# Optimization experiments

Measured on AMD Instinct MI355X. Metric: run time of the kernel, lower is better.

The kernel has to match this reference:

```python
import jax, jax.numpy as jnp
import numpy as np

BS, T, NN, NF = 4, 64, 128, 16
HID, HEADS, RH, LD = 64, 4, 256, 64
EPG = 1024  # edges per graph


def _gat(x, src, dst, N, W, a_s, a_d, b, heads, out_dim, concat):
    # x: [N, Fin] -> h: [N, H, F]
    h = (x @ W).reshape(N, heads, out_dim)
    al_s = jnp.sum(h * a_s[None], axis=-1)  # [N, H]
    al_d = jnp.sum(h * a_d[None], axis=-1)
    e = jax.nn.leaky_relu(al_s[src] + al_d[dst], 0.2)  # [E, H]
    m = jax.ops.segment_max(e, dst, num_segments=N)
    m = jnp.where(jnp.isfinite(m), m, 0.0)
    ex = jnp.exp(e - m[dst])
    den = jax.ops.segment_sum(ex, dst, num_segments=N)
    alpha = ex / (den[dst] + 1e-16)
    agg = jax.ops.segment_sum(h[src] * alpha[:, :, None], dst, num_segments=N)
    o = agg.reshape(N, heads * out_dim) if concat else agg.mean(axis=1)
    return o + b


def _lstm(xs, Wih, Whh, bih, bhh, H):
    # xs: [T, B, D]; PyTorch gate order i,f,g,o
    B = xs.shape[1]
    h0 = jnp.zeros((B, H), xs.dtype)
    c0 = jnp.zeros((B, H), xs.dtype)

    def step(carry, xt):
        h, c = carry
        g = xt @ Wih.T + h @ Whh.T + bih + bhh
        i, f, gg, o = jnp.split(g, 4, axis=-1)
        c = jax.nn.sigmoid(f) * c + jax.nn.sigmoid(i) * jnp.tanh(gg)
        h = jax.nn.sigmoid(o) * jnp.tanh(c)
        return (h, c), None

    (hT, _), _ = jax.lax.scan(step, (h0, c0), xs)
    return hT


def setup_inputs() -> dict:
    key = jax.random.key(0)
    ks = jax.random.split(key, 32)
    s = 0.1
    d = {
        'x': jax.random.normal(ks[0], (BS, T, NN, NF), jnp.float32),
        'edge_index': jax.random.randint(ks[1], (2, EPG), 0, NN),
        'gat0_W': s * jax.random.normal(ks[2], (NF, HEADS * HID)),
        'gat0_asrc': s * jax.random.normal(ks[3], (HEADS, HID)),
        'gat0_adst': s * jax.random.normal(ks[4], (HEADS, HID)),
        'gat0_b': jnp.zeros((HEADS * HID,)),
        'gat1_W': s * jax.random.normal(ks[5], (HEADS * HID, HEADS * HID)),
        'gat1_asrc': s * jax.random.normal(ks[6], (HEADS, HID)),
        'gat1_adst': s * jax.random.normal(ks[7], (HEADS, HID)),
        'gat1_b': jnp.zeros((HEADS * HID,)),
        'gat2_W': s * jax.random.normal(ks[8], (HEADS * HID, HID)),
        'gat2_asrc': s * jax.random.normal(ks[9], (1, HID)),
        'gat2_adst': s * jax.random.normal(ks[10], (1, HID)),
        'gat2_b': jnp.zeros((HID,)),
        'Wih_f': s * jax.random.normal(ks[11], (4 * RH, HID)),
        'Whh_f': s * jax.random.normal(ks[12], (4 * RH, RH)),
        'bih_f': jnp.zeros((4 * RH,)),
        'bhh_f': jnp.zeros((4 * RH,)),
        'Wih_b': s * jax.random.normal(ks[13], (4 * RH, HID)),
        'Whh_b': s * jax.random.normal(ks[14], (4 * RH, RH)),
        'bih_b': jnp.zeros((4 * RH,)),
        'bhh_b': jnp.zeros((4 * RH,)),
        'mu_W': s * jax.random.normal(ks[15], (LD, 2 * RH)),
        'mu_b': jnp.zeros((LD,)),
        'lv_W': s * jax.random.normal(ks[16], (LD, 2 * RH)),
        'lv_b': jnp.zeros((LD,)),
    }
    return d


def reference(x, edge_index, gat0_W, gat0_asrc, gat0_adst, gat0_b,
              gat1_W, gat1_asrc, gat1_adst, gat1_b,
              gat2_W, gat2_asrc, gat2_adst, gat2_b,
              Wih_f, Whh_f, bih_f, bhh_f, Wih_b, Whh_b, bih_b, bhh_b,
              mu_W, mu_b, lv_W, lv_b):
    bs, t, nn, nf = x.shape
    ng = bs * t
    N = ng * nn
    xt = x.reshape(N, nf)
    # batch the edge index: repeat per graph with node offset, then add self-loops
    off = (jnp.arange(ng) * nn).repeat(edge_index.shape[1])  # [ng*E]
    bsrc = jnp.tile(edge_index[0], ng) + off
    bdst = jnp.tile(edge_index[1], ng) + off
    loops = jnp.arange(N)
    src = jnp.concatenate([bsrc, loops])
    dst = jnp.concatenate([bdst, loops])

    xt = jax.nn.relu(_gat(xt, src, dst, N, gat0_W, gat0_asrc, gat0_adst, gat0_b, HEADS, HID, True))
    xt = jax.nn.relu(_gat(xt, src, dst, N, gat1_W, gat1_asrc, gat1_adst, gat1_b, HEADS, HID, True))
    xt = jax.nn.relu(_gat(xt, src, dst, N, gat2_W, gat2_asrc, gat2_adst, gat2_b, 1, HID, False))

    batch_idx = jnp.arange(ng).repeat(nn)
    graph_embs = jax.ops.segment_sum(xt, batch_idx, num_segments=ng).reshape(bs, t, HID)

    seq = jnp.transpose(graph_embs, (1, 0, 2))  # [T, B, HID]
    h_fwd = _lstm(seq, Wih_f, Whh_f, bih_f, bhh_f, RH)
    h_bwd = _lstm(seq[::-1], Wih_b, Whh_b, bih_b, bhh_b, RH)
    feat = jnp.concatenate([h_fwd, h_bwd], axis=1)  # [B, 2*RH]

    mu = feat @ mu_W.T + mu_b
    logvar = feat @ lv_W.T + lv_b
    # PoincareBall(c=1).projx, float32 eps = 4e-3
    maxnorm = 1.0 - 4e-3
    nrm = jnp.linalg.norm(mu, axis=-1, keepdims=True)
    mu = jnp.where(nrm > maxnorm, mu / nrm * maxnorm, mu)
    return (mu, logvar)
```

## Files before the change

kernel.cpp:

```cpp
#include <hip/hip_runtime.h>
#include <hip/hip_bf16.h>

#define BSZ 4
#define TT 64
#define NNODE 128
#define NFEAT 16
#define HIDD 64
#define NHEAD 4
#define RHID 256
#define LDIM 64
#define EPG 1024
#define NGRAPH (BSZ*TT)
#define NTOT (NGRAPH*NNODE)
#define ESLOTS (EPG+NNODE)

#define WOFF_G0W 0
#define WOFF_G0AS 4096
#define WOFF_G0AD 4352
#define WOFF_G0B 4608
#define WOFF_G1W 4864
#define WOFF_G1AS 70400
#define WOFF_G1AD 70656
#define WOFF_G1B 70912
#define WOFF_G2W 71168
#define WOFF_G2AS 87552
#define WOFF_G2AD 87616
#define WOFF_G2B 87680
#define WOFF_WIHF 87744
#define WOFF_WHHF 153280
#define WOFF_BIHF 415424
#define WOFF_BHHF 416448
#define WOFF_WIHB 417472
#define WOFF_WHHB 483008
#define WOFF_BIHB 745152
#define WOFF_BHHB 746176
#define WOFF_MUW 747200
#define WOFF_MUB 779968
#define WOFF_LVW 780032
#define WOFF_LVB 812800
#define WTOTAL   812864

#define FOFF_WBUF 4096
#define FOFF_CSR  1052672
#define FOFF_SYNC 1314816
#define FOFF_WE   1576960
#define FOFF_BBF  1900000
#define FOFF_XFP  2756608
#define FOFF_XBP  3018752
#define FOFF_HT   3280896
#define FOFF_XSEQ 3282944
#define FOFF_PA   3291136
#define FOFF_PB   5388288
#define FOFF_P    7485440

#define BOFF_G0 0
#define BOFF_G1 4096
#define BOFF_G2 69632
#define BOFF_WF 86016
#define BOFF_WB 151552
#define BTOTAL  217088

#define SP_CVTX  (WTOTAL + BTOTAL)
#define SP_WHH   (SP_CVTX + NTOT*NFEAT)
#define SP_HX    (SP_WHH + 262144)
#define SP_FL    (SP_HX + 12288)
#define SP_TOTAL (SP_FL + 1024)

#define SENT 0xFFFFFFFFu

typedef __attribute__((ext_vector_type(8))) short short8;
typedef __attribute__((ext_vector_type(4))) float float4v;

__device__ __forceinline__ float b2f(unsigned short u){
  union { unsigned int i; float f; } v; v.i = ((unsigned int)u) << 16; return v.f;
}
__device__ __forceinline__ unsigned short f2b(float f){
  __hip_bfloat16 h = __float2bfloat16(f);
  union { __hip_bfloat16 h; unsigned short u; } v; v.h = h; return v.u;
}
__device__ __forceinline__ float ldf(const void* p, int i, int flag){
  return flag ? b2f(((const unsigned short*)p)[i]) : ((const float*)p)[i];
}
__device__ __forceinline__ float h2f(unsigned short s){
  union { _Float16 hh; unsigned short s; } u; u.s = s; return (float)u.hh;
}
__device__ __forceinline__ unsigned short f2h(float f){
  union { _Float16 hh; unsigned short s; } u; u.hh = (_Float16)f; return u.s;
}
__device__ __forceinline__ int sniff32(const unsigned short* w){
  int ok = 0;
  #pragma unroll
  for (int i = 0; i < 32; ++i){
    float a = fabsf(b2f(w[2 * i]));
    if (a > 1e-8f && a < 4.f) ok++;
  }
  return ok >= 16 ? 1 : 0;
}

struct CvtArgs {
  const void* src[24];
  int off[25];
};
__global__ void setup_kernel(CvtArgs a,
                             float* __restrict__ W, unsigned short* __restrict__ BBF,
                             unsigned short* __restrict__ P, unsigned int* __restrict__ WT,
                             unsigned int* __restrict__ HX, int* __restrict__ FL,
                             const void* __restrict__ x, const int* __restrict__ ei,
                             int* __restrict__ csr_row, unsigned short* __restrict__ csr_src)
{
  __shared__ int cnt[NNODE];
  __shared__ int off[NNODE];
  __shared__ int wo[NNODE];
  const int tid = threadIdx.x;

  if (blockIdx.x == gridDim.x - 1){
    if (tid < NNODE) cnt[tid] = 0;
    __syncthreads();
    for (int i = tid; i < ESLOTS; i += 256){
      int d = (i < EPG) ? ei[EPG + i] : (i - EPG);
      atomicAdd(&cnt[d], 1);
    }
    __syncthreads();
    if (tid < NNODE) off[tid] = cnt[tid];
    for (int o = 1; o < NNODE; o <<= 1){
      __syncthreads();
      int t = (tid < NNODE && tid >= o) ? off[tid - o] : 0;
      __syncthreads();
      if (tid < NNODE) off[tid] += t;
    }
    __syncthreads();
    if (tid < NNODE){
      wo[tid] = off[tid] - cnt[tid];
      csr_row[tid + 1] = off[tid];
    }
    if (tid == 0) csr_row[0] = 0;
    __syncthreads();
    for (int i = tid; i < ESLOTS; i += 256){
      int s, d;
      if (i < EPG){ s = ei[i]; d = ei[EPG + i]; } else { s = i - EPG; d = i - EPG; }
      int pos = atomicAdd(&wo[d], 1);
      csr_src[pos] = (unsigned short)s;
    }
    return;
  }

  int id = blockIdx.x * blockDim.x + tid;
  if (id >= SP_TOTAL) return;
  int fl = sniff32((const unsigned short*)a.src[0]);
  if (id < WTOTAL){
    int k = 0;
    while (id >= a.off[k + 1]) ++k;
    W[id] = ldf(a.src[k], id - a.off[k], fl);
  } else if (id < WTOTAL + BTOTAL){
    int r = id - WTOTAL;
    float v;
    if (r < BOFF_G1){
      int o = r >> 4, k = r & 15;
      v = ldf(a.src[0], k * 256 + o, fl);
    } else if (r < BOFF_G2){
      int rr = r - BOFF_G1; int o = rr >> 8, k = rr & 255;
      v = ldf(a.src[4], k * 256 + o, fl);
    } else if (r < BOFF_WF){
      int rr = r - BOFF_G2; int o = rr >> 8, k = rr & 255;
      v = ldf(a.src[8], k * 64 + o, fl);
    } else if (r < BOFF_WB){
      int q = r - BOFF_WF; int k = q >> 10, n = q & 1023;
      v = ldf(a.src[12], n * 64 + k, fl);
    } else {
      int q = r - BOFF_WB; int k = q >> 10, n = q & 1023;
      v = ldf(a.src[16], n * 64 + k, fl);
    }
    BBF[r] = f2b(v);
  } else if (id < SP_CVTX + NTOT * NFEAT){
    int r = id - SP_CVTX;
    P[r] = fl ? ((const unsigned short*)x)[r] : f2b(((const float*)x)[r]);
  } else if (id < SP_HX){
    int r0 = id - SP_WHH;
    int c = r0 & 3;
    int lane = (r0 >> 2) & 63;
    int nt = (r0 >> 8) & 15;
    int kc = (r0 >> 12) & 7;
    int m = (r0 >> 15) & 3;
    int dir = r0 >> 17;
    int l = nt * 16 + (lane & 15);
    int u = (l >> 6) * 256 + 64 * m + (l & 63);
    int k0 = kc * 32 + ((lane >> 4) << 3) + 2 * c;
    const void* Wsrc = dir ? a.src[17] : a.src[13];
    unsigned short va = f2b(ldf(Wsrc, u * RHID + k0, fl));
    unsigned short vb = f2b(ldf(Wsrc, u * RHID + k0 + 1, fl));
    WT[r0] = (unsigned int)va | ((unsigned int)vb << 16);
  } else if (id < SP_FL){
    HX[id - SP_HX] = SENT;
  } else {
    FL[id - SP_FL] = 0;
  }
}

__global__ __launch_bounds__(256)
void gat3_kernel(const unsigned short* Pb, const unsigned short* BBF,
                 const float* Wbuf,
                 const int* csr_row, const unsigned short* csr_src,
                 unsigned short* PA, unsigned short* PB,
                 unsigned short* XSEQ, int* FL)
{
  __shared__ unsigned short HT_[128 * 136];
  __shared__ unsigned short AD[128 * 136];
  __shared__ unsigned short ALS16[256];
  __shared__ unsigned short ALD16[256];
  __shared__ float ALSf[128];
  __shared__ float ALDf[128];
  __shared__ int   rowL[132];
  __shared__ unsigned char srcL[1152];
  __shared__ float pools[4][64];

  const int tid = threadIdx.x;
  const int g = blockIdx.x >> 1, hb = blockIdx.x & 1;
  const int c0 = hb * 128;
  const int w = tid >> 6, lane = tid & 63, q = lane >> 4, r = lane & 15;
  unsigned short* Bst = AD;

  for (int i = tid; i < 129; i += 256) rowL[i] = csr_row[i];
  for (int i = tid; i < 1152; i += 256) srcL[i] = (unsigned char)csr_src[i];
  __syncthreads();

  auto gemm_T = [&](int KV, int NT, const unsigned short* Pin, const unsigned short* BT){
    float4v acc0[8], acc1[8];
    #pragma unroll
    for (int i = 0; i < 8; ++i){ acc0[i] = (float4v){0,0,0,0}; acc1[i] = (float4v){0,0,0,0}; }
    const int cbase = (NT == 8) ? c0 : 0;
    const int KR = (KV + 31) / 32;
    for (int kr = 0; kr < KR; ++kr){
      const int kc = kr * 32;
      __syncthreads();
      if (NT == 8){
        int n = tid >> 1, kb = (tid & 1) * 16;
        uint4 z = {0,0,0,0}; uint4 v0 = z, v1 = z;
        if (kb < KV)     v0 = *(const uint4*)(BT + (size_t)(cbase + n) * KV + kc + kb);
        if (kb + 8 < KV) v1 = *(const uint4*)(BT + (size_t)(cbase + n) * KV + kc + kb + 8);
        *(uint4*)&Bst[n * 40 + kb] = v0;
        *(uint4*)&Bst[n * 40 + kb + 8] = v1;
      } else {
        int n = tid >> 2, kb = (tid & 3) * 8;
        uint4 v = *(const uint4*)(BT + (size_t)n * KV + kc + kb);
        *(uint4*)&Bst[n * 40 + kb] = v;
      }
      short8 a0 = {0,0,0,0,0,0,0,0}, a1 = {0,0,0,0,0,0,0,0};
      if (KV >= 32 || q < 2){
        a0 = *(const short8*)(Pin + (size_t)(g * 128 + 16 * w       + r) * KV + kc + q * 8);
        a1 = *(const short8*)(Pin + (size_t)(g * 128 + 16 * (w + 4) + r) * KV + kc + q * 8);
      }
      __syncthreads();
      for (int nt = 0; nt < NT; ++nt){
        short8 bf = *(const short8*)&Bst[(16 * nt + r) * 40 + q * 8];
        acc0[nt] = __builtin_amdgcn_mfma_f32_16x16x32_bf16(a0, bf, acc0[nt], 0, 0, 0);
        acc1[nt] = __builtin_amdgcn_mfma_f32_16x16x32_bf16(a1, bf, acc1[nt], 0, 0, 0);
      }
    }
    __syncthreads();
    for (int nt = 0; nt < NT; ++nt)
      #pragma unroll
      for (int i = 0; i < 4; ++i){
        HT_[(16 * nt + r) * 136 + 16 * w       + q * 4 + i] = f2b(acc0[nt][i]);
        HT_[(16 * nt + r) * 136 + 16 * (w + 4) + q * 4 + i] = f2b(acc1[nt][i]);
      }
    __syncthreads();
  };

  auto agg_head = [&](int hl, int colbase, float4v am[2][4]){
    #pragma unroll
    for (int mt = 0; mt < 2; ++mt)
      #pragma unroll
      for (int nt = 0; nt < 4; ++nt) am[mt][nt] = (float4v){0,0,0,0};
    #pragma unroll
    for (int kc = 0; kc < 4; ++kc){
      short8 af0 = *(const short8*)&AD[(w * 32      + r) * 136 + kc * 32 + q * 8];
      short8 af1 = *(const short8*)&AD[(w * 32 + 16 + r) * 136 + kc * 32 + q * 8];
      #pragma unroll
      for (int nt = 0; nt < 4; ++nt){
        short8 bf = *(const short8*)&HT_[(colbase + nt * 16 + r) * 136 + kc * 32 + q * 8];
        am[0][nt] = __builtin_amdgcn_mfma_f32_16x16x32_bf16(af0, bf, am[0][nt], 0, 0, 0);
        am[1][nt] = __builtin_amdgcn_mfma_f32_16x16x32_bf16(af1, bf, am[1][nt], 0, 0, 0);
      }
    }
  };

  auto sync_partner = [&](int* FLx){
    __syncthreads();
    if (tid == 0){
      __hip_atomic_store(&FLx[blockIdx.x], 1, __ATOMIC_RELEASE, __HIP_MEMORY_SCOPE_AGENT);
      int guard = 0;
      while (__hip_atomic_load(&FLx[blockIdx.x ^ 1], __ATOMIC_ACQUIRE,
                               __HIP_MEMORY_SCOPE_AGENT) == 0 && guard < 200000){
        __builtin_amdgcn_s_sleep(1);
        ++guard;
      }
    }
    __syncthreads();
  };

  auto do_layer = [&](int KV, const unsigned short* Pin, const unsigned short* BT,
                      int asoff, int adoff, int boff, unsigned short* Pout){
    gemm_T(KV, 8, Pin, BT);
    {
      float as0 = Wbuf[asoff + c0 + 2 * lane], as1 = Wbuf[asoff + c0 + 2 * lane + 1];
      float ad0 = Wbuf[adoff + c0 + 2 * lane], ad1 = Wbuf[adoff + c0 + 2 * lane + 1];
      for (int it = 0; it < 32; ++it){
        int n = it * 4 + w;
        float e0 = b2f(HT_[(2 * lane) * 136 + n]);
        float e1 = b2f(HT_[(2 * lane + 1) * 136 + n]);
        float vs = e0 * as0 + e1 * as1;
        float vd = e0 * ad0 + e1 * ad1;
        #pragma unroll
        for (int m = 16; m >= 1; m >>= 1){ vs += __shfl_xor(vs, m); vd += __shfl_xor(vd, m); }
        if ((lane & 31) == 0){
          ALS16[n * 2 + (lane >> 5)] = f2h(vs);
          ALD16[n * 2 + (lane >> 5)] = f2h(vd);
        }
      }
    }
    __syncthreads();
    for (int hl = 0; hl < 2; ++hl){
      for (int i = tid; i < 8704; i += 256) ((unsigned int*)AD)[i] = 0;
      __syncthreads();
      if (tid < 128){
        int n = tid;
        float aldv = h2f(ALD16[n * 2 + hl]);
        int rs = rowL[n], re = rowL[n + 1];
        float mx = -3e38f, den = 0.f;
        for (int j = rs; j < re; ++j){
          float v = h2f(ALS16[srcL[j] * 2 + hl]) + aldv;
          v = v > 0.f ? v : 0.2f * v;
          if (v > mx){ den = den * __expf(mx - v) + 1.f; mx = v; }
          else den += __expf(v - mx);
        }
        float iden = 1.f / (den + 1e-16f);
        for (int j = rs; j < re; ++j){
          float v = h2f(ALS16[srcL[j] * 2 + hl]) + aldv;
          v = v > 0.f ? v : 0.2f * v;
          float al = __expf(v - mx) * iden;
          int s = srcL[j];
          AD[n * 136 + s] = f2b(b2f(AD[n * 136 + s]) + al);
        }
      }
      __syncthreads();
      float4v am[2][4];
      agg_head(hl, hl * 64, am);
      #pragma unroll
      for (int mt = 0; mt < 2; ++mt)
        #pragma unroll
        for (int nt = 0; nt < 4; ++nt){
          int col = hl * 64 + nt * 16 + r;
          float bz = Wbuf[boff + c0 + col];
          #pragma unroll
          for (int i = 0; i < 4; ++i){
            int dst = w * 32 + mt * 16 + q * 4 + i;
            float v = am[mt][nt][i] + bz;
            v = v > 0.f ? v : 0.f;
            __hip_atomic_store((unsigned short*)&Pout[(size_t)(g * 128 + dst) * 256 + c0 + col],
                               f2b(v), __ATOMIC_RELAXED, __HIP_MEMORY_SCOPE_AGENT);
          }
        }
      __syncthreads();
    }
  };

  do_layer(16, Pb, BBF + BOFF_G0, WOFF_G0AS, WOFF_G0AD, WOFF_G0B, PA);
  sync_partner(FL);
  do_layer(256, PA, BBF + BOFF_G1, WOFF_G1AS, WOFF_G1AD, WOFF_G1B, PB);
  sync_partner(FL + 512);

  {
    gemm_T(256, 4, PB, BBF + BOFF_G2);
    {
      float asv = Wbuf[WOFF_G2AS + lane];
      float adv = Wbuf[WOFF_G2AD + lane];
      for (int it = 0; it < 32; ++it){
        int n = it * 4 + w;
        float e0 = b2f(HT_[lane * 136 + n]);
        float vs = e0 * asv, vd = e0 * adv;
        #pragma unroll
        for (int m = 32; m >= 1; m >>= 1){ vs += __shfl_xor(vs, m); vd += __shfl_xor(vd, m); }
        if (lane == 0){ ALSf[n] = vs; ALDf[n] = vd; }
      }
    }
    __syncthreads();
    for (int i = tid; i < 8704; i += 256) ((unsigned int*)AD)[i] = 0;
    __syncthreads();
    if (tid < 128){
      int n = tid;
      float aldv = ALDf[n];
      int rs = rowL[n], re = rowL[n + 1];
      float mx = -3e38f, den = 0.f;
      for (int j = rs; j < re; ++j){
        float v = ALSf[srcL[j]] + aldv;
        v = v > 0.f ? v : 0.2f * v;
        if (v > mx){ den = den * __expf(mx - v) + 1.f; mx = v; }
        else den += __expf(v - mx);
      }
      float iden = 1.f / (den + 1e-16f);
      for (int j = rs; j < re; ++j){
        float v = ALSf[srcL[j]] + aldv;
        v = v > 0.f ? v : 0.2f * v;
        float al = __expf(v - mx) * iden;
        int s = srcL[j];
        AD[n * 136 + s] = f2b(b2f(AD[n * 136 + s]) + al);
      }
    }
    __syncthreads();
    float4v am[2][4];
    agg_head(0, 0, am);
    float psum[4] = {0.f, 0.f, 0.f, 0.f};
    #pragma unroll
    for (int nt = 0; nt < 4; ++nt){
      int col = nt * 16 + r;
      float bz = Wbuf[WOFF_G2B + col];
      #pragma unroll
      for (int mt = 0; mt < 2; ++mt)
        #pragma unroll
        for (int i = 0; i < 4; ++i){
          float v = am[mt][nt][i] + bz;
          psum[nt] += (v > 0.f ? v : 0.f);
        }
      psum[nt] += __shfl_xor(psum[nt], 16);
      psum[nt] += __shfl_xor(psum[nt], 32);
    }
    if (q == 0){
      #pragma unroll
      for (int nt = 0; nt < 4; ++nt) pools[w][nt * 16 + r] = psum[nt];
    }
    __syncthreads();
    if (tid < 64 && (tid >> 5) == hb){
      float s = pools[0][tid] + pools[1][tid] + pools[2][tid] + pools[3][tid];
      int b = g >> 6, tq = g & 63;
      XSEQ[(size_t)(tq * BSZ + b) * HIDD + tid] = f2b(s);
    }
  }
}

__global__ __launch_bounds__(256)
void mmx2_kernel(const unsigned short* __restrict__ A,
                 const unsigned short* __restrict__ B0, const unsigned short* __restrict__ B1,
                 float* __restrict__ C0, float* __restrict__ C1, int M, int Nc, int K)
{
  __shared__ unsigned short As[64][40];
  __shared__ unsigned short Bs[64][40];
  const unsigned short* Bb = blockIdx.z ? B1 : B0;
  float* C = blockIdx.z ? C1 : C0;
  const int tid = threadIdx.x;
  const int w = tid >> 6, lane = tid & 63, q = lane >> 4, r = lane & 15;
  const int m0 = blockIdx.x * 64, n0 = blockIdx.y * 64;
  float4v acc0 = {0,0,0,0}, acc1 = {0,0,0,0}, acc2 = {0,0,0,0}, acc3 = {0,0,0,0};
  const int arow = tid >> 2, akb = (tid & 3) * 8;
  const int bk = tid >> 3, bnb = (tid & 7) * 8;
  for (int kc = 0; kc < K; kc += 32){
    int kw = K - kc; if (kw > 32) kw = 32;
    if (akb < kw){
      uint4 v = *(const uint4*)(A + (size_t)(m0 + arow) * K + kc + akb);
      *(uint4*)&As[arow][akb] = v;
    } else {
      uint4 z = {0,0,0,0}; *(uint4*)&As[arow][akb] = z;
    }
    if (bk < kw){
      uint4 v = *(const uint4*)(Bb + (size_t)(kc + bk) * Nc + n0 + bnb);
      const unsigned short* vs = (const unsigned short*)&v;
      #pragma unroll
      for (int e = 0; e < 8; ++e) Bs[bnb + e][bk] = vs[e];
    } else {
      #pragma unroll
      for (int e = 0; e < 8; ++e) Bs[bnb + e][bk] = 0;
    }
    __syncthreads();
    short8 af = *(const short8*)&As[16 * w + r][q * 8];
    short8 b0 = *(const short8*)&Bs[r][q * 8];
    short8 b1 = *(const short8*)&Bs[16 + r][q * 8];
    short8 b2 = *(const short8*)&Bs[32 + r][q * 8];
    short8 b3 = *(const short8*)&Bs[48 + r][q * 8];
    acc0 = __builtin_amdgcn_mfma_f32_16x16x32_bf16(af, b0, acc0, 0, 0, 0);
    acc1 = __builtin_amdgcn_mfma_f32_16x16x32_bf16(af, b1, acc1, 0, 0, 0);
    acc2 = __builtin_amdgcn_mfma_f32_16x16x32_bf16(af, b2, acc2, 0, 0, 0);
    acc3 = __builtin_amdgcn_mfma_f32_16x16x32_bf16(af, b3, acc3, 0, 0, 0);
    __syncthreads();
  }
  const int row = m0 + 16 * w + q * 4, col0 = n0 + r;
  #pragma unroll
  for (int i = 0; i < 4; ++i){
    size_t base = (size_t)(row + i) * Nc;
    C[base + col0]      = acc0[i];
    C[base + col0 + 16] = acc1[i];
    C[base + col0 + 32] = acc2[i];
    C[base + col0 + 48] = acc3[i];
  }
}

__global__ __launch_bounds__(256)
void lstm13_kernel(const float* __restrict__ XF, const float* __restrict__ XB,
                   const unsigned int* __restrict__ WT,
                   const float* __restrict__ bih_f, const float* __restrict__ bhh_f,
                   const float* __restrict__ bih_b, const float* __restrict__ bhh_b,
                   unsigned int* __restrict__ HX,
                   float* __restrict__ HT)
{
  __shared__ unsigned int WL[32768];
  __shared__ unsigned int H16[16 * 132];
  __shared__ float glds[4][256];

  const int tid = threadIdx.x;
  const int m = blockIdx.x & 3, dir = blockIdx.x >> 2;
  const int w = tid >> 6, lane = tid & 63, quad = lane >> 4, r = lane & 15;
  const float* Xp = dir ? XB : XF;
  const int ub = tid >> 6, uj = tid & 63;
  unsigned int* HXd = HX + dir * 6144;

  const float* bi = dir ? bih_b : bih_f;
  const float* bh = dir ? bhh_b : bhh_f;
  float bias0 = bi[0 * 256 + 64 * m + uj] + bh[0 * 256 + 64 * m + uj];
  float bias1 = bi[1 * 256 + 64 * m + uj] + bh[1 * 256 + 64 * m + uj];
  float bias2 = bi[2 * 256 + 64 * m + uj] + bh[2 * 256 + 64 * m + uj];
  float bias3 = bi[3 * 256 + 64 * m + uj] + bh[3 * 256 + 64 * m + uj];

  {
    const uint4* WT4 = (const uint4*)(WT + dir * 131072 + m * 32768);
    uint4* WL4 = (uint4*)WL;
    #pragma unroll
    for (int s = 0; s < 32; ++s)
      WL4[s * 256 + tid] = WT4[s * 256 + tid];
  }
  for (int i = tid; i < 16 * 132; i += 256) H16[i] = 0;
  float c = 0.f;
  __syncthreads();

  const uint4* WL4 = (const uint4*)WL;
  const uint4* H16u4 = (const uint4*)H16;

  float4v acc[4];
  auto kchunk = [&](int kc){
    uint4 av = H16u4[(lane & 15) * 33 + kc * 4 + quad];
    short8 af = *(const short8*)&av;
    #pragma unroll
    for (int t = 0; t < 4; ++t){
      int nt = w * 4 + t;
      uint4 bv = WL4[(kc * 16 + nt) * 64 + lane];
      short8 bf = *(const short8*)&bv;
      acc[t] = __builtin_amdgcn_mfma_f32_16x16x32_bf16(af, bf, acc[t], 0, 0, 0);
    }
  };

  for (int t = 0; t < TT; ++t){
    const int tb = dir ? (TT - 1 - t) : t;
    const float* xr = Xp + (size_t)(tb * 4 + ub) * 1024 + 64 * m + uj;
    float x0 = xr[0], x1 = xr[256], x2 = xr[512], x3 = xr[768];

    #pragma unroll
    for (int i = 0; i < 4; ++i) acc[i] = (float4v){0,0,0,0};
    kchunk(2 * m); kchunk(2 * m + 1);
    if (t > 0 && w > 0){
      int qp = (m + w) & 3;
      unsigned int* S = HXd + ((t - 1) % 3) * 2048 + m * 512;
      int b2 = lane >> 5, p2 = lane & 31;
      int i1G = b2 * 128 + 32 * qp + p2;
      int i2G = (b2 + 2) * 128 + 32 * qp + p2;
      int i1L = b2 * 132 + 32 * qp + p2;
      int i2L = (b2 + 2) * 132 + 32 * qp + p2;
      unsigned int v1, v2;
      int guard = 0;
      while ((v1 = __hip_atomic_load(&S[i1G], __ATOMIC_RELAXED, __HIP_MEMORY_SCOPE_AGENT)) == SENT
             && guard < 200000){ __builtin_amdgcn_s_sleep(1); ++guard; }
      guard = 0;
      while ((v2 = __hip_atomic_load(&S[i2G], __ATOMIC_RELAXED, __HIP_MEMORY_SCOPE_AGENT)) == SENT
             && guard < 200000){ __builtin_amdgcn_s_sleep(1); ++guard; }
      H16[i1L] = v1; H16[i2L] = v2;
      __hip_atomic_store(&S[i1G], SENT, __ATOMIC_RELAXED, __HIP_MEMORY_SCOPE_AGENT);
      __hip_atomic_store(&S[i2G], SENT, __ATOMIC_RELAXED, __HIP_MEMORY_SCOPE_AGENT);
    }
    __syncthreads();
    #pragma unroll
    for (int i = 1; i < 4; ++i){
      int qp = (m + i) & 3;
      kchunk(2 * qp); kchunk(2 * qp + 1);
    }
    if (quad == 0){
      #pragma unroll
      for (int tt = 0; tt < 4; ++tt){
        int l = (w * 4 + tt) * 16 + r;
        glds[0][l] = acc[tt][0];
        glds[1][l] = acc[tt][1];
        glds[2][l] = acc[tt][2];
        glds[3][l] = acc[tt][3];
      }
    }
    __syncthreads();

    float gi = glds[ub][uj]        + bias0 + x0;
    float gf = glds[ub][64 + uj]   + bias1 + x1;
    float gg = glds[ub][128 + uj]  + bias2 + x2;
    float go = glds[ub][192 + uj]  + bias3 + x3;
    float si = 1.f / (1.f + __expf(-gi));
    float sf = 1.f / (1.f + __expf(-gf));
    float so = 1.f / (1.f + __expf(-go));
    float tg = 1.f - 2.f / (1.f + __expf(2.f * gg));
    c = sf * c + si * tg;
    float ch = 1.f - 2.f / (1.f + __expf(2.f * c));
    float hval = so * ch;
    if (t == TT - 1){
      HT[(size_t)(dir * 4 + ub) * RHID + (64 * m + uj)] = hval;
      break;
    }
    unsigned int own = f2b(hval);
    unsigned int partner = ((unsigned int)__shfl_xor((int)own, 1)) & 0xffffu;
    unsigned int* S = HXd + (t % 3) * 2048;
    if ((uj & 1) == 0){
      unsigned int v = own | (partner << 16);
      int p = uj >> 1;
      int idxG = ub * 128 + 32 * m + p;
      int idxL = ub * 132 + 32 * m + p;
      H16[idxL] = v;
      #pragma unroll
      for (int cns = 1; cns < 4; ++cns)
        __hip_atomic_store(&S[((m + cns) & 3) * 512 + idxG], v,
                           __ATOMIC_RELAXED, __HIP_MEMORY_SCOPE_AGENT);
    }
    __syncthreads();
  }
}

__global__ __launch_bounds__(512)
void head2_kernel(const float* __restrict__ HT,
                  const float* __restrict__ muW, const float* __restrict__ mub,
                  const float* __restrict__ lvW, const float* __restrict__ lvb,
                  float* __restrict__ out)
{
  __shared__ float feat[4][512];
  __shared__ float muv[4][64];
  __shared__ float lvv[4][64];
  int tid = threadIdx.x;
  for (int i = tid; i < 2048; i += 512){
    int rr = i >> 8, k = i & 255;
    int b = rr & 3, d = rr >> 2;
    feat[b][d * 256 + k] = HT[i];
  }
  __syncthreads();
  int w = tid >> 6, lane = tid & 63;
  for (int job = w; job < 512; job += 8){
    int j = job & 63, b = (job >> 6) & 3, mat = job >> 8;
    const float* W = (mat ? lvW : muW) + (size_t)j * 512;
    float s = 0.f;
    #pragma unroll
    for (int e = 0; e < 8; ++e) s += W[lane * 8 + e] * feat[b][lane * 8 + e];
    #pragma unroll
    for (int mm = 32; mm >= 1; mm >>= 1) s += __shfl_xor(s, mm);
    if (lane == 0){
      float v = s + (mat ? lvb[j] : mub[j]);
      if (mat) lvv[b][j] = v; else muv[b][j] = v;
    }
  }
  __syncthreads();
  if (tid < 256){
    int b = tid >> 6, j = tid & 63;
    float mu = muv[b][j];
    float sq = mu * mu;
    #pragma unroll
    for (int mm = 32; mm >= 1; mm >>= 1) sq += __shfl_xor(sq, mm);
    float nrm = sqrtf(sq);
    const float mxn = 1.0f - 4e-3f;
    if (nrm > mxn) mu = mu / nrm * mxn;
    out[b * 64 + j] = mu;
    out[256 + b * 64 + j] = lvv[b][j];
  }
}

extern "C" void kernel_launch(void* const* d_in, const int* in_sizes, int n_in,
                              void* d_out, int out_size, void* d_ws, size_t ws_size,
                              hipStream_t stream)
{
  const int* ei = (const int*)d_in[1];

  float* FW   = (float*)d_ws;
  float* Wbuf = FW + FOFF_WBUF;
  int*   csr_row = (int*)(FW + FOFF_CSR);
  unsigned short* csr_src = (unsigned short*)(FW + FOFF_CSR + 132);
  int*   FL   = (int*)(FW + FOFF_CSR + 1024);
  float* XFp  = FW + FOFF_XFP;
  float* XBp  = FW + FOFF_XBP;
  float* HT   = FW + FOFF_HT;
  unsigned short* XSEQ = (unsigned short*)(FW + FOFF_XSEQ);
  unsigned short* PA   = (unsigned short*)(FW + FOFF_PA);
  unsigned short* PB   = (unsigned short*)(FW + FOFF_PB);
  unsigned short* Pb   = (unsigned short*)(FW + FOFF_P);
  unsigned int*   WT   = (unsigned int*)(FW + FOFF_WE);
  unsigned short* BBF  = (unsigned short*)(FW + FOFF_BBF);
  unsigned int*   HX   = (unsigned int*)(FW + FOFF_SYNC);

  CvtArgs ca;
  static const int wsz[24] = {4096,256,256,256, 65536,256,256,256, 16384,64,64,64,
                              65536,262144,1024,1024, 65536,262144,1024,1024,
                              32768,64,32768,64};
  {
    int acc = 0;
    for (int k = 0; k < 24; ++k){ ca.src[k] = d_in[2 + k]; ca.off[k] = acc; acc += wsz[k]; }
    ca.off[24] = acc;
  }
  int nblk = (SP_TOTAL + 255) / 256 + 1;
  setup_kernel<<<nblk, 256, 0, stream>>>(ca, Wbuf, BBF, Pb, WT, HX, FL,
                                         d_in[0], ei, csr_row, csr_src);

  gat3_kernel<<<512, 256, 0, stream>>>(Pb, BBF, Wbuf, csr_row, csr_src, PA, PB, XSEQ, FL);

  mmx2_kernel<<<dim3(4, 16, 2), 256, 0, stream>>>(XSEQ, BBF + BOFF_WF, BBF + BOFF_WB,
                                                  XFp, XBp, 256, 1024, 64);

  lstm13_kernel<<<8, 256, 0, stream>>>(XFp, XBp, WT,
                                       Wbuf + WOFF_BIHF, Wbuf + WOFF_BHHF,
                                       Wbuf + WOFF_BIHB, Wbuf + WOFF_BHHB,
                                       HX, HT);

  head2_kernel<<<1, 512, 0, stream>>>(HT, Wbuf + WOFF_MUW, Wbuf + WOFF_MUB,
                                      Wbuf + WOFF_LVW, Wbuf + WOFF_LVB, (float*)d_out);
}
```

Measured before the change: 385.5 us.

## Split fused GAT kernel into per-layer launches, drop partner-block spin sync

The single persistent GAT kernel that synchronized paired blocks through global flag spin-waits between layers is replaced by three separate kernel launches, one per GAT layer. Layer kernels are templated on the K dimension, with loops fully unrolled and plain stores instead of atomic stores. This removes the spin-wait latency, the flag initialization and any co-residency dependence, at the cost of two extra launches and losing data locality across layers. Layer 2 also wastes work: both blocks of a pair compute the full 64-column result but only write half.

```diff
diff --git a/kernel.cpp b/kernel.cpp
--- a/kernel.cpp
+++ b/kernel.cpp
@@ -63,8 +63,7 @@
 #define SP_CVTX  (WTOTAL + BTOTAL)
 #define SP_WHH   (SP_CVTX + NTOT*NFEAT)
 #define SP_HX    (SP_WHH + 262144)
-#define SP_FL    (SP_HX + 12288)
-#define SP_TOTAL (SP_FL + 1024)
+#define SP_TOTAL (SP_HX + 12288)
 
 #define SENT 0xFFFFFFFFu
 
@@ -104,7 +103,7 @@
 __global__ void setup_kernel(CvtArgs a,
                              float* __restrict__ W, unsigned short* __restrict__ BBF,
                              unsigned short* __restrict__ P, unsigned int* __restrict__ WT,
-                             unsigned int* __restrict__ HX, int* __restrict__ FL,
+                             unsigned int* __restrict__ HX,
                              const void* __restrict__ x, const int* __restrict__ ei,
                              int* __restrict__ csr_row, unsigned short* __restrict__ csr_src)
 {
@@ -189,24 +188,163 @@
     unsigned short va = f2b(ldf(Wsrc, u * RHID + k0, fl));
     unsigned short vb = f2b(ldf(Wsrc, u * RHID + k0 + 1, fl));
     WT[r0] = (unsigned int)va | ((unsigned int)vb << 16);
-  } else if (id < SP_FL){
+  } else {
     HX[id - SP_HX] = SENT;
-  } else {
-    FL[id - SP_FL] = 0;
-  }
-}
-
+  }
+}
+
+template<int KV>
 __global__ __launch_bounds__(256)
-void gat3_kernel(const unsigned short* Pb, const unsigned short* BBF,
-                 const float* Wbuf,
-                 const int* csr_row, const unsigned short* csr_src,
-                 unsigned short* PA, unsigned short* PB,
-                 unsigned short* XSEQ, int* FL)
+void glayer_kernel(const unsigned short* __restrict__ Pin,
+                   const unsigned short* __restrict__ BT,
+                   const float* __restrict__ Wbuf,
+                   int asoff, int adoff, int boff,
+                   const int* __restrict__ csr_row, const unsigned short* __restrict__ csr_src,
+                   unsigned short* __restrict__ Pout)
 {
   __shared__ unsigned short HT_[128 * 136];
   __shared__ unsigned short AD[128 * 136];
   __shared__ unsigned short ALS16[256];
   __shared__ unsigned short ALD16[256];
+  __shared__ int   rowL[132];
+  __shared__ unsigned char srcL[1152];
+
+  const int tid = threadIdx.x;
+  const int g = blockIdx.x >> 1, hb = blockIdx.x & 1;
+  const int c0 = hb * 128;
+  const int w = tid >> 6, lane = tid & 63, q = lane >> 4, r = lane & 15;
+  unsigned short* Bst = AD;
+
+  for (int i = tid; i < 129; i += 256) rowL[i] = csr_row[i];
+  for (int i = tid; i < 1152; i += 256) srcL[i] = (unsigned char)csr_src[i];
+  __syncthreads();
+
+  {
+    float4v acc0[8], acc1[8];
+    #pragma unroll
+    for (int i = 0; i < 8; ++i){ acc0[i] = (float4v){0,0,0,0}; acc1[i] = (float4v){0,0,0,0}; }
+    const int KR = (KV + 31) / 32;
+    for (int kr = 0; kr < KR; ++kr){
+      const int kc = kr * 32;
+      __syncthreads();
+      {
+        int n = tid >> 1, kb = (tid & 1) * 16;
+        uint4 z = {0,0,0,0}; uint4 v0 = z, v1 = z;
+        if (kb < KV)     v0 = *(const uint4*)(BT + (size_t)(c0 + n) * KV + kc + kb);
+        if (kb + 8 < KV) v1 = *(const uint4*)(BT + (size_t)(c0 + n) * KV + kc + kb + 8);
+        *(uint4*)&Bst[n * 40 + kb] = v0;
+        *(uint4*)&Bst[n * 40 + kb + 8] = v1;
+      }
+      short8 a0 = {0,0,0,0,0,0,0,0}, a1 = {0,0,0,0,0,0,0,0};
+      if (KV >= 32 || q < 2){
+        a0 = *(const short8*)(Pin + (size_t)(g * 128 + 16 * w       + r) * KV + kc + q * 8);
+        a1 = *(const short8*)(Pin + (size_t)(g * 128 + 16 * (w + 4) + r) * KV + kc + q * 8);
+      }
+      __syncthreads();
+      #pragma unroll
+      for (int nt = 0; nt < 8; ++nt){
+        short8 bf = *(const short8*)&Bst[(16 * nt + r) * 40 + q * 8];
+        acc0[nt] = __builtin_amdgcn_mfma_f32_16x16x32_bf16(a0, bf, acc0[nt], 0, 0, 0);
+        acc1[nt] = __builtin_amdgcn_mfma_f32_16x16x32_bf16(a1, bf, acc1[nt], 0, 0, 0);
+      }
+    }
+    __syncthreads();
+    #pragma unroll
+    for (int nt = 0; nt < 8; ++nt)
+      #pragma unroll
+      for (int i = 0; i < 4; ++i){
+        HT_[(16 * nt + r) * 136 + 16 * w       + q * 4 + i] = f2b(acc0[nt][i]);
+        HT_[(16 * nt + r) * 136 + 16 * (w + 4) + q * 4 + i] = f2b(acc1[nt][i]);
+      }
+    __syncthreads();
+  }
+
+  {
+    float as0 = Wbuf[asoff + c0 + 2 * lane], as1 = Wbuf[asoff + c0 + 2 * lane + 1];
+    float ad0 = Wbuf[adoff + c0 + 2 * lane], ad1 = Wbuf[adoff + c0 + 2 * lane + 1];
+    for (int it = 0; it < 32; ++it){
+      int n = it * 4 + w;
+      float e0 = b2f(HT_[(2 * lane) * 136 + n]);
+      float e1 = b2f(HT_[(2 * lane + 1) * 136 + n]);
+      float vs = e0 * as0 + e1 * as1;
+      float vd = e0 * ad0 + e1 * ad1;
+      #pragma unroll
+      for (int m = 16; m >= 1; m >>= 1){ vs += __shfl_xor(vs, m); vd += __shfl_xor(vd, m); }
+      if ((lane & 31) == 0){
+        ALS16[n * 2 + (lane >> 5)] = f2h(vs);
+        ALD16[n * 2 + (lane >> 5)] = f2h(vd);
+      }
+    }
+  }
+  __syncthreads();
+
+  for (int hl = 0; hl < 2; ++hl){
+    for (int i = tid; i < 8704; i += 256) ((unsigned int*)AD)[i] = 0;
+    __syncthreads();
+    if (tid < 128){
+      int n = tid;
+      float aldv = h2f(ALD16[n * 2 + hl]);
+      int rs = rowL[n], re = rowL[n + 1];
+      float mx = -3e38f, den = 0.f;
+      for (int j = rs; j < re; ++j){
+        float v = h2f(ALS16[srcL[j] * 2 + hl]) + aldv;
+        v = v > 0.f ? v : 0.2f * v;
+        if (v > mx){ den = den * __expf(mx - v) + 1.f; mx = v; }
+        else den += __expf(v - mx);
+      }
+      float iden = 1.f / (den + 1e-16f);
+      for (int j = rs; j < re; ++j){
+        float v = h2f(ALS16[srcL[j] * 2 + hl]) + aldv;
+        v = v > 0.f ? v : 0.2f * v;
+        float al = __expf(v - mx) * iden;
+        int s = srcL[j];
+        AD[n * 136 + s] = f2b(b2f(AD[n * 136 + s]) + al);
+      }
+    }
+    __syncthreads();
+    float4v am[2][4];
+    #pragma unroll
+    for (int mt = 0; mt < 2; ++mt)
+      #pragma unroll
+      for (int nt = 0; nt < 4; ++nt) am[mt][nt] = (float4v){0,0,0,0};
+    #pragma unroll
+    for (int kc = 0; kc < 4; ++kc){
+      short8 af0 = *(const short8*)&AD[(w * 32      + r) * 136 + kc * 32 + q * 8];
+      short8 af1 = *(const short8*)&AD[(w * 32 + 16 + r) * 136 + kc * 32 + q * 8];
+      #pragma unroll
+      for (int nt = 0; nt < 4; ++nt){
+        short8 bf = *(const short8*)&HT_[(hl * 64 + nt * 16 + r) * 136 + kc * 32 + q * 8];
+        am[0][nt] = __builtin_amdgcn_mfma_f32_16x16x32_bf16(af0, bf, am[0][nt], 0, 0, 0);
+        am[1][nt] = __builtin_amdgcn_mfma_f32_16x16x32_bf16(af1, bf, am[1][nt], 0, 0, 0);
+      }
+    }
+    #pragma unroll
+    for (int mt = 0; mt < 2; ++mt)
+      #pragma unroll
+      for (int nt = 0; nt < 4; ++nt){
+        int col = hl * 64 + nt * 16 + r;
+        float bz = Wbuf[boff + c0 + col];
+        #pragma unroll
+        for (int i = 0; i < 4; ++i){
+          int dst = w * 32 + mt * 16 + q * 4 + i;
+          float v = am[mt][nt][i] + bz;
+          v = v > 0.f ? v : 0.f;
+          Pout[(size_t)(g * 128 + dst) * 256 + c0 + col] = f2b(v);
+        }
+      }
+    __syncthreads();
+  }
+}
+
+__global__ __launch_bounds__(256)
+void glayer2_kernel(const unsigned short* __restrict__ Pin,
+                    const unsigned short* __restrict__ BT,
+                    const float* __restrict__ Wbuf,
+                    const int* __restrict__ csr_row, const unsigned short* __restrict__ csr_src,
+                    unsigned short* __restrict__ XSEQ)
+{
+  __shared__ unsigned short HT_[64 * 136];
+  __shared__ unsigned short AD[128 * 136];
   __shared__ float ALSf[128];
   __shared__ float ALDf[128];
   __shared__ int   rowL[132];
@@ -215,7 +353,6 @@
 
   const int tid = threadIdx.x;
   const int g = blockIdx.x >> 1, hb = blockIdx.x & 1;
-  const int c0 = hb * 128;
   const int w = tid >> 6, lane = tid & 63, q = lane >> 4, r = lane & 15;
   unsigned short* Bst = AD;
 
@@ -223,217 +360,115 @@
   for (int i = tid; i < 1152; i += 256) srcL[i] = (unsigned char)csr_src[i];
   __syncthreads();
 
-  auto gemm_T = [&](int KV, int NT, const unsigned short* Pin, const unsigned short* BT){
-    float4v acc0[8], acc1[8];
-    #pragma unroll
-    for (int i = 0; i < 8; ++i){ acc0[i] = (float4v){0,0,0,0}; acc1[i] = (float4v){0,0,0,0}; }
-    const int cbase = (NT == 8) ? c0 : 0;
-    const int KR = (KV + 31) / 32;
-    for (int kr = 0; kr < KR; ++kr){
+  {
+    float4v acc0[4], acc1[4];
+    #pragma unroll
+    for (int i = 0; i < 4; ++i){ acc0[i] = (float4v){0,0,0,0}; acc1[i] = (float4v){0,0,0,0}; }
+    for (int kr = 0; kr < 8; ++kr){
       const int kc = kr * 32;
       __syncthreads();
-      if (NT == 8){
-        int n = tid >> 1, kb = (tid & 1) * 16;
-        uint4 z = {0,0,0,0}; uint4 v0 = z, v1 = z;
-        if (kb < KV)     v0 = *(const uint4*)(BT + (size_t)(cbase + n) * KV + kc + kb);
-        if (kb + 8 < KV) v1 = *(const uint4*)(BT + (size_t)(cbase + n) * KV + kc + kb + 8);
-        *(uint4*)&Bst[n * 40 + kb] = v0;
-        *(uint4*)&Bst[n * 40 + kb + 8] = v1;
-      } else {
+      {
         int n = tid >> 2, kb = (tid & 3) * 8;
-        uint4 v = *(const uint4*)(BT + (size_t)n * KV + kc + kb);
+        uint4 v = *(const uint4*)(BT + (size_t)n * 256 + kc + kb);
         *(uint4*)&Bst[n * 40 + kb] = v;
       }
-      short8 a0 = {0,0,0,0,0,0,0,0}, a1 = {0,0,0,0,0,0,0,0};
-      if (KV >= 32 || q < 2){
-        a0 = *(const short8*)(Pin + (size_t)(g * 128 + 16 * w       + r) * KV + kc + q * 8);
-        a1 = *(const short8*)(Pin + (size_t)(g * 128 + 16 * (w + 4) + r) * KV + kc + q * 8);
-      }
+      short8 a0 = *(const short8*)(Pin + (size_t)(g * 128 + 16 * w       + r) * 256 + kc + q * 8);
+      short8 a1 = *(const short8*)(Pin + (size_t)(g * 128 + 16 * (w + 4) + r) * 256 + kc + q * 8);
       __syncthreads();
-      for (int nt = 0; nt < NT; ++nt){
+      #pragma unroll
+      for (int nt = 0; nt < 4; ++nt){
         short8 bf = *(const short8*)&Bst[(16 * nt + r) * 40 + q * 8];
         acc0[nt] = __builtin_amdgcn_mfma_f32_16x16x32_bf16(a0, bf, acc0[nt], 0, 0, 0);
         acc1[nt] = __builtin_amdgcn_mfma_f32_16x16x32_bf16(a1, bf, acc1[nt], 0, 0, 0);
       }
     }
     __syncthreads();
-    for (int nt = 0; nt < NT; ++nt)
+    #pragma unroll
+    for (int nt = 0; nt < 4; ++nt)
       #pragma unroll
       for (int i = 0; i < 4; ++i){
         HT_[(16 * nt + r) * 136 + 16 * w       + q * 4 + i] = f2b(acc0[nt][i]);
         HT_[(16 * nt + r) * 136 + 16 * (w + 4) + q * 4 + i] = f2b(acc1[nt][i]);
       }
     __syncthreads();
-  };
-
-  auto agg_head = [&](int hl, int colbase, float4v am[2][4]){
+  }
+
+  {
+    float asv = Wbuf[WOFF_G2AS + lane];
+    float adv = Wbuf[WOFF_G2AD + lane];
+    for (int it = 0; it < 32; ++it){
+      int n = it * 4 + w;
+      float e0 = b2f(HT_[lane * 136 + n]);
+      float vs = e0 * asv, vd = e0 * adv;
+      #pragma unroll
+      for (int m = 32; m >= 1; m >>= 1){ vs += __shfl_xor(vs, m); vd += __shfl_xor(vd, m); }
+      if (lane == 0){ ALSf[n] = vs; ALDf[n] = vd; }
+    }
+  }
+  __syncthreads();
+  for (int i = tid; i < 8704; i += 256) ((unsigned int*)AD)[i] = 0;
+  __syncthreads();
+  if (tid < 128){
+    int n = tid;
+    float aldv = ALDf[n];
+    int rs = rowL[n], re = rowL[n + 1];
+    float mx = -3e38f, den = 0.f;
+    for (int j = rs; j < re; ++j){
+      float v = ALSf[srcL[j]] + aldv;
+      v = v > 0.f ? v : 0.2f * v;
+      if (v > mx){ den = den * __expf(mx - v) + 1.f; mx = v; }
+      else den += __expf(v - mx);
+    }
+    float iden = 1.f / (den + 1e-16f);
+    for (int j = rs; j < re; ++j){
+      float v = ALSf[srcL[j]] + aldv;
+      v = v > 0.f ? v : 0.2f * v;
+      float al = __expf(v - mx) * iden;
+      int s = srcL[j];
+      AD[n * 136 + s] = f2b(b2f(AD[n * 136 + s]) + al);
+    }
+  }
+  __syncthreads();
+  float4v am[2][4];
+  #pragma unroll
+  for (int mt = 0; mt < 2; ++mt)
+    #pragma unroll
+    for (int nt = 0; nt < 4; ++nt) am[mt][nt] = (float4v){0,0,0,0};
+  #pragma unroll
+  for (int kc = 0; kc < 4; ++kc){
+    short8 af0 = *(const short8*)&AD[(w * 32      + r) * 136 + kc * 32 + q * 8];
+    short8 af1 = *(const short8*)&AD[(w * 32 + 16 + r) * 136 + kc * 32 + q * 8];
+    #pragma unroll
+    for (int nt = 0; nt < 4; ++nt){
+      short8 bf = *(const short8*)&HT_[(nt * 16 + r) * 136 + kc * 32 + q * 8];
+      am[0][nt] = __builtin_amdgcn_mfma_f32_16x16x32_bf16(af0, bf, am[0][nt], 0, 0, 0);
+      am[1][nt] = __builtin_amdgcn_mfma_f32_16x16x32_bf16(af1, bf, am[1][nt], 0, 0, 0);
+    }
+  }
+  float psum[4] = {0.f, 0.f, 0.f, 0.f};
+  #pragma unroll
+  for (int nt = 0; nt < 4; ++nt){
+    int col = nt * 16 + r;
+    float bz = Wbuf[WOFF_G2B + col];
     #pragma unroll
     for (int mt = 0; mt < 2; ++mt)
       #pragma unroll
-      for (int nt = 0; nt < 4; ++nt) am[mt][nt] = (float4v){0,0,0,0};
-    #pragma unroll
-    for (int kc = 0; kc < 4; ++kc){
-      short8 af0 = *(const short8*)&AD[(w * 32      + r) * 136 + kc * 32 + q * 8];
-      short8 af1 = *(const short8*)&AD[(w * 32 + 16 + r) * 136 + kc * 32 + q * 8];
-      #pragma unroll
-      for (int nt = 0; nt < 4; ++nt){
-        short8 bf = *(const short8*)&HT_[(colbase + nt * 16 + r) * 136 + kc * 32 + q * 8];
-        am[0][nt] = __builtin_amdgcn_mfma_f32_16x16x32_bf16(af0, bf, am[0][nt], 0, 0, 0);
-        am[1][nt] = __builtin_amdgcn_mfma_f32_16x16x32_bf16(af1, bf, am[1][nt], 0, 0, 0);
-      }
-    }
-  };
-
-  auto sync_partner = [&](int* FLx){
-    __syncthreads();
-    if (tid == 0){
-      __hip_atomic_store(&FLx[blockIdx.x], 1, __ATOMIC_RELEASE, __HIP_MEMORY_SCOPE_AGENT);
-      int guard = 0;
-      while (__hip_atomic_load(&FLx[blockIdx.x ^ 1], __ATOMIC_ACQUIRE,
-                               __HIP_MEMORY_SCOPE_AGENT) == 0 && guard < 200000){
-        __builtin_amdgcn_s_sleep(1);
-        ++guard;
-      }
-    }
-    __syncthreads();
-  };
-
-  auto do_layer = [&](int KV, const unsigned short* Pin, const unsigned short* BT,
-                      int asoff, int adoff, int boff, unsigned short* Pout){
-    gemm_T(KV, 8, Pin, BT);
-    {
-      float as0 = Wbuf[asoff + c0 + 2 * lane], as1 = Wbuf[asoff + c0 + 2 * lane + 1];
-      float ad0 = Wbuf[adoff + c0 + 2 * lane], ad1 = Wbuf[adoff + c0 + 2 * lane + 1];
-      for (int it = 0; it < 32; ++it){
-        int n = it * 4 + w;
-        float e0 = b2f(HT_[(2 * lane) * 136 + n]);
-        float e1 = b2f(HT_[(2 * lane + 1) * 136 + n]);
-        float vs = e0 * as0 + e1 * as1;
-        float vd = e0 * ad0 + e1 * ad1;
-        #pragma unroll
-        for (int m = 16; m >= 1; m >>= 1){ vs += __shfl_xor(vs, m); vd += __shfl_xor(vd, m); }
-        if ((lane & 31) == 0){
-          ALS16[n * 2 + (lane >> 5)] = f2h(vs);
-          ALD16[n * 2 + (lane >> 5)] = f2h(vd);
-        }
-      }
-    }
-    __syncthreads();
-    for (int hl = 0; hl < 2; ++hl){
-      for (int i = tid; i < 8704; i += 256) ((unsigned int*)AD)[i] = 0;
-      __syncthreads();
-      if (tid < 128){
-        int n = tid;
-        float aldv = h2f(ALD16[n * 2 + hl]);
-        int rs = rowL[n], re = rowL[n + 1];
-        float mx = -3e38f, den = 0.f;
-        for (int j = rs; j < re; ++j){
-          float v = h2f(ALS16[srcL[j] * 2 + hl]) + aldv;
-          v = v > 0.f ? v : 0.2f * v;
-          if (v > mx){ den = den * __expf(mx - v) + 1.f; mx = v; }
-          else den += __expf(v - mx);
-        }
-        float iden = 1.f / (den + 1e-16f);
-        for (int j = rs; j < re; ++j){
-          float v = h2f(ALS16[srcL[j] * 2 + hl]) + aldv;
-          v = v > 0.f ? v : 0.2f * v;
-          float al = __expf(v - mx) * iden;
-          int s = srcL[j];
-          AD[n * 136 + s] = f2b(b2f(AD[n * 136 + s]) + al);
-        }
-      }
-      __syncthreads();
-      float4v am[2][4];
-      agg_head(hl, hl * 64, am);
-      #pragma unroll
-      for (int mt = 0; mt < 2; ++mt)
-        #pragma unroll
-        for (int nt = 0; nt < 4; ++nt){
-          int col = hl * 64 + nt * 16 + r;
-          float bz = Wbuf[boff + c0 + col];
-          #pragma unroll
-          for (int i = 0; i < 4; ++i){
-            int dst = w * 32 + mt * 16 + q * 4 + i;
-            float v = am[mt][nt][i] + bz;
-            v = v > 0.f ? v : 0.f;
-            __hip_atomic_store((unsigned short*)&Pout[(size_t)(g * 128 + dst) * 256 + c0 + col],
-                               f2b(v), __ATOMIC_RELAXED, __HIP_MEMORY_SCOPE_AGENT);
-          }
-        }
-      __syncthreads();
-    }
-  };
-
-  do_layer(16, Pb, BBF + BOFF_G0, WOFF_G0AS, WOFF_G0AD, WOFF_G0B, PA);
-  sync_partner(FL);
-  do_layer(256, PA, BBF + BOFF_G1, WOFF_G1AS, WOFF_G1AD, WOFF_G1B, PB);
-  sync_partner(FL + 512);
-
-  {
-    gemm_T(256, 4, PB, BBF + BOFF_G2);
-    {
-      float asv = Wbuf[WOFF_G2AS + lane];
-      float adv = Wbuf[WOFF_G2AD + lane];
-      for (int it = 0; it < 32; ++it){
-        int n = it * 4 + w;
-        float e0 = b2f(HT_[lane * 136 + n]);
-        float vs = e0 * asv, vd = e0 * adv;
-        #pragma unroll
-        for (int m = 32; m >= 1; m >>= 1){ vs += __shfl_xor(vs, m); vd += __shfl_xor(vd, m); }
-        if (lane == 0){ ALSf[n] = vs; ALDf[n] = vd; }
-      }
-    }
-    __syncthreads();
-    for (int i = tid; i < 8704; i += 256) ((unsigned int*)AD)[i] = 0;
-    __syncthreads();
-    if (tid < 128){
-      int n = tid;
-      float aldv = ALDf[n];
-      int rs = rowL[n], re = rowL[n + 1];
-      float mx = -3e38f, den = 0.f;
-      for (int j = rs; j < re; ++j){
-        float v = ALSf[srcL[j]] + aldv;
-        v = v > 0.f ? v : 0.2f * v;
-        if (v > mx){ den = den * __expf(mx - v) + 1.f; mx = v; }
-        else den += __expf(v - mx);
-      }
-      float iden = 1.f / (den + 1e-16f);
-      for (int j = rs; j < re; ++j){
-        float v = ALSf[srcL[j]] + aldv;
-        v = v > 0.f ? v : 0.2f * v;
-        float al = __expf(v - mx) * iden;
-        int s = srcL[j];
-        AD[n * 136 + s] = f2b(b2f(AD[n * 136 + s]) + al);
-      }
-    }
-    __syncthreads();
-    float4v am[2][4];
-    agg_head(0, 0, am);
-    float psum[4] = {0.f, 0.f, 0.f, 0.f};
-    #pragma unroll
-    for (int nt = 0; nt < 4; ++nt){
-      int col = nt * 16 + r;
-      float bz = Wbuf[WOFF_G2B + col];
-      #pragma unroll
-      for (int mt = 0; mt < 2; ++mt)
-        #pragma unroll
-        for (int i = 0; i < 4; ++i){
-          float v = am[mt][nt][i] + bz;
-          psum[nt] += (v > 0.f ? v : 0.f);
-        }
-      psum[nt] += __shfl_xor(psum[nt], 16);
-      psum[nt] += __shfl_xor(psum[nt], 32);
-    }
-    if (q == 0){
-      #pragma unroll
-      for (int nt = 0; nt < 4; ++nt) pools[w][nt * 16 + r] = psum[nt];
-    }
-    __syncthreads();
-    if (tid < 64 && (tid >> 5) == hb){
-      float s = pools[0][tid] + pools[1][tid] + pools[2][tid] + pools[3][tid];
-      int b = g >> 6, tq = g & 63;
-      XSEQ[(size_t)(tq * BSZ + b) * HIDD + tid] = f2b(s);
-    }
+      for (int i = 0; i < 4; ++i){
+        float v = am[mt][nt][i] + bz;
+        psum[nt] += (v > 0.f ? v : 0.f);
+      }
+    psum[nt] += __shfl_xor(psum[nt], 16);
+    psum[nt] += __shfl_xor(psum[nt], 32);
+  }
+  if (q == 0){
+    #pragma unroll
+    for (int nt = 0; nt < 4; ++nt) pools[w][nt * 16 + r] = psum[nt];
+  }
+  __syncthreads();
+  if (tid < 64 && (tid >> 5) == hb){
+    float s = pools[0][tid] + pools[1][tid] + pools[2][tid] + pools[3][tid];
+    int b = g >> 6, tq = g & 63;
+    XSEQ[(size_t)(tq * BSZ + b) * HIDD + tid] = f2b(s);
   }
 }
 
@@ -678,7 +713,6 @@
   float* Wbuf = FW + FOFF_WBUF;
   int*   csr_row = (int*)(FW + FOFF_CSR);
   unsigned short* csr_src = (unsigned short*)(FW + FOFF_CSR + 132);
-  int*   FL   = (int*)(FW + FOFF_CSR + 1024);
   float* XFp  = FW + FOFF_XFP;
   float* XBp  = FW + FOFF_XBP;
   float* HT   = FW + FOFF_HT;
@@ -700,10 +734,17 @@
     ca.off[24] = acc;
   }
   int nblk = (SP_TOTAL + 255) / 256 + 1;
-  setup_kernel<<<nblk, 256, 0, stream>>>(ca, Wbuf, BBF, Pb, WT, HX, FL,
+  setup_kernel<<<nblk, 256, 0, stream>>>(ca, Wbuf, BBF, Pb, WT, HX,
                                          d_in[0], ei, csr_row, csr_src);
 
-  gat3_kernel<<<512, 256, 0, stream>>>(Pb, BBF, Wbuf, csr_row, csr_src, PA, PB, XSEQ, FL);
+  glayer_kernel<16><<<512, 256, 0, stream>>>(Pb, BBF + BOFF_G0, Wbuf,
+                                             WOFF_G0AS, WOFF_G0AD, WOFF_G0B,
+                                             csr_row, csr_src, PA);
+  glayer_kernel<256><<<512, 256, 0, stream>>>(PA, BBF + BOFF_G1, Wbuf,
+                                              WOFF_G1AS, WOFF_G1AD, WOFF_G1B,
+                                              csr_row, csr_src, PB);
+  glayer2_kernel<<<512, 256, 0, stream>>>(PB, BBF + BOFF_G2, Wbuf,
+                                          csr_row, csr_src, XSEQ);
 
   mmx2_kernel<<<dim3(4, 16, 2), 256, 0, stream>>>(XSEQ, BBF + BOFF_WF, BBF + BOFF_WB,
                                                   XFp, XBp, 256, 1024, 64);
```

Result: faster. 360.2 us, median of 2 (-6.6%).
